# Kernel tuning notes

Measured on AMD Instinct MI355X. Metric: run time of the kernel, lower is better.

The kernel has to match this reference:

```python
import jax, jax.numpy as jnp
import numpy as np

VOCAB, EMB, HID, MAXLEN, BATCH = 32000, 256, 512, 64, 64


def setup_inputs() -> dict:
    key = jax.random.key(0)
    ks = jax.random.split(key, 12)
    s_e = 1.0 / np.sqrt(EMB)
    s_h = 1.0 / np.sqrt(HID)
    return {
        "encoder_h": jax.random.normal(ks[0], (1, BATCH, HID), jnp.float32),
        "encoder_c": jax.random.normal(ks[1], (1, BATCH, HID), jnp.float32),
        "target": jax.random.randint(ks[2], (BATCH, MAXLEN), 0, VOCAB, jnp.int64),
        "tf_mask": jax.random.randint(ks[3], (MAXLEN,), 0, 2, jnp.int32),
        "embedding": jax.random.normal(ks[4], (VOCAB, EMB), jnp.float32),
        "w_ih": jax.random.normal(ks[5], (4 * HID, EMB), jnp.float32) * s_e,
        "w_hh": jax.random.normal(ks[6], (4 * HID, HID), jnp.float32) * s_h,
        "b_ih": jax.random.normal(ks[7], (4 * HID,), jnp.float32) * s_h,
        "b_hh": jax.random.normal(ks[8], (4 * HID,), jnp.float32) * s_h,
        "fc_w": jax.random.normal(ks[9], (VOCAB, HID), jnp.float32) * s_h,
        "fc_b": jax.random.normal(ks[10], (VOCAB,), jnp.float32) * s_h,
        "target_length": 64,
    }


def reference(encoder_h, encoder_c, target, tf_mask, embedding, w_ih, w_hh,
              b_ih, b_hh, fc_w, fc_b, target_length):
    # encoder_h/c: [num_layers=1, B, H]; target: [B, T]; tf_mask: [T] (1 -> teacher forcing)
    B = target.shape[0]
    h0, c0 = encoder_h[0], encoder_c[0]              # [B, H]
    inp0 = jnp.zeros((B,), jnp.int32)                # SOS token id 0
    bias = b_ih + b_hh

    def step(carry, xs):
        h, c, inp = carry
        tgt_t, tf_t = xs
        x = embedding[inp]                           # [B, E] lookup
        gates = x @ w_ih.T + h @ w_hh.T + bias       # [B, 4H], PyTorch gate order i,f,g,o
        i, f, g, o = jnp.split(gates, 4, axis=-1)
        i, f, o = jax.nn.sigmoid(i), jax.nn.sigmoid(f), jax.nn.sigmoid(o)
        c = f * c + i * jnp.tanh(g)
        h = o * jnp.tanh(c)
        logits = h @ fc_w.T + fc_b                   # [B, V]
        greedy = jnp.argmax(logits, axis=-1).astype(jnp.int32)  # top-1 decode
        nxt = jnp.where(tf_t > 0, tgt_t, greedy)     # teacher forcing vs. greedy
        return (h, c, nxt), logits

    tgt_seq = target.T.astype(jnp.int32)             # [T, B]
    (h, c, _), outs = jax.lax.scan(step, (h0, c0, inp0), (tgt_seq, tf_mask))
    decoder_outputs = jnp.transpose(outs, (1, 0, 2))  # [B, T, V]
    return decoder_outputs, h[None], c[None]
```

## Files before the change

### kernel.cpp

```cpp
#include <hip/hip_runtime.h>
#include <cstdint>

#define VOCAB  32000
#define EMB    256
#define HID    512
#define TLEN   64
#define BATCH  64
#define G4     2048
#define OUT_LOGITS ((size_t)BATCH * TLEN * VOCAB)
#define BTV    ((size_t)TLEN * VOCAB)

typedef short s16x8 __attribute__((ext_vector_type(8)));
typedef float f32x4 __attribute__((ext_vector_type(4)));

#define WS_FCW_HI  0ull
#define WS_FCW_LO  32768000ull
#define WS_WIH_HI  65536000ull
#define WS_WIH_LO  66584576ull
#define WS_WHH_HI  67633152ull
#define WS_WHH_LO  69730304ull
#define WS_BIAS    71827456ull
#define WS_CBUF    71835648ull
#define WS_HBUF    71966720ull
#define WS_HHI     72097792ull
#define WS_HLO     76357632ull
#define WS_AMAX    80617472ull
#define WS_NEEDED  80650240ull

__device__ __forceinline__ unsigned bf16_hi_bits(float x) {
    unsigned u = __float_as_uint(x);
    return (u + 0x7FFFu + ((u >> 16) & 1u)) >> 16;
}
__device__ __forceinline__ float bf16_bits_to_f(unsigned b) {
    return __uint_as_float(b << 16);
}
__device__ __forceinline__ unsigned fkey(float x) {
    unsigned u = __float_as_uint(x);
    return (u & 0x80000000u) ? ~u : (u | 0x80000000u);
}

__global__ __launch_bounds__(256) void k_pre(
    const float* __restrict__ fcw, const float* __restrict__ wih, const float* __restrict__ whh,
    const float* __restrict__ bih, const float* __restrict__ bhh,
    const float* __restrict__ ench, const float* __restrict__ encc,
    unsigned short* fcw_hi, unsigned short* fcw_lo,
    unsigned short* wih_hi, unsigned short* wih_lo,
    unsigned short* whh_hi, unsigned short* whh_lo,
    float* bias, float* c_buf, unsigned short* hhi, unsigned short* hlo,
    unsigned long long* amax)
{
    size_t g = (size_t)blockIdx.x * 256 + threadIdx.x;
    size_t s = (size_t)gridDim.x * 256;
    for (size_t i = g; i < (size_t)VOCAB * HID; i += s) {
        float x = fcw[i]; unsigned hb = bf16_hi_bits(x);
        fcw_hi[i] = (unsigned short)hb;
        fcw_lo[i] = (unsigned short)bf16_hi_bits(x - bf16_bits_to_f(hb));
    }
    for (size_t i = g; i < (size_t)G4 * EMB; i += s) {
        float x = wih[i]; unsigned hb = bf16_hi_bits(x);
        wih_hi[i] = (unsigned short)hb;
        wih_lo[i] = (unsigned short)bf16_hi_bits(x - bf16_bits_to_f(hb));
    }
    for (size_t i = g; i < (size_t)G4 * HID; i += s) {
        float x = whh[i]; unsigned hb = bf16_hi_bits(x);
        whh_hi[i] = (unsigned short)hb;
        whh_lo[i] = (unsigned short)bf16_hi_bits(x - bf16_bits_to_f(hb));
    }
    for (size_t i = g; i < G4; i += s) bias[i] = bih[i] + bhh[i];
    for (size_t i = g; i < (size_t)BATCH * HID; i += s) {
        c_buf[i] = encc[i];
        float x = ench[i]; unsigned hb = bf16_hi_bits(x);
        hhi[i] = (unsigned short)hb;
        hlo[i] = (unsigned short)bf16_hi_bits(x - bf16_bits_to_f(hb));
    }
    for (size_t i = g; i < (size_t)TLEN * BATCH; i += s) amax[i] = 0ull;
}

__global__ __launch_bounds__(256) void k_cell(
    const float* __restrict__ emb,
    const unsigned short* __restrict__ wih_hi, const unsigned short* __restrict__ wih_lo,
    const unsigned short* __restrict__ whh_hi, const unsigned short* __restrict__ whh_lo,
    const float* __restrict__ bias,
    const int* __restrict__ target, const int* __restrict__ tf_mask,
    const unsigned long long* __restrict__ amax,
    float* c_buf, float* h_buf, unsigned short* hhi, unsigned short* hlo, int t)
{
    __shared__ __align__(16) unsigned short xs_hi[16 * 264];
    __shared__ __align__(16) unsigned short xs_lo[16 * 264];
    __shared__ float gbuf[4 * 16 * 16];
    __shared__ int tok_s[16];

    const int tid = threadIdx.x;
    const int jt = blockIdx.x >> 2;
    const int b0 = (blockIdx.x & 3) * 16;

    if (tid < 16) {
        int b = b0 + tid;
        int tok = 0;
        if (t > 0) {
            if (tf_mask[t - 1] > 0) tok = target[b * TLEN + (t - 1)];
            else {
                unsigned long long k = amax[(size_t)(t - 1) * BATCH + b];
                tok = (int)(~(unsigned)k);
            }
        }
        tok_s[tid] = tok;
    }
    __syncthreads();

    for (int i = tid; i < 16 * 32; i += 256) {
        int row = i >> 5, seg = i & 31;
        const float* src = emb + (size_t)tok_s[row] * EMB + seg * 8;
        int dst = row * 264 + seg * 8;
        #pragma unroll
        for (int e = 0; e < 8; e++) {
            float x = src[e]; unsigned hb = bf16_hi_bits(x);
            xs_hi[dst + e] = (unsigned short)hb;
            xs_lo[dst + e] = (unsigned short)bf16_hi_bits(x - bf16_bits_to_f(hb));
        }
    }
    __syncthreads();

    const int w = tid >> 6, l = tid & 63, li = l & 15, q = l >> 4;
    const int row0 = w * HID + jt * 16;
    const unsigned short* hh = hhi + (size_t)t * BATCH * HID;
    const unsigned short* hl = hlo + (size_t)t * BATCH * HID;

    f32x4 acc = {0.f, 0.f, 0.f, 0.f};
    #pragma unroll
    for (int kc = 0; kc < 8; kc++) {
        int ka = kc * 32 + q * 8;
        s16x8 ah = *(const s16x8*)(wih_hi + (size_t)(row0 + li) * EMB + ka);
        s16x8 al = *(const s16x8*)(wih_lo + (size_t)(row0 + li) * EMB + ka);
        s16x8 bh = *(const s16x8*)(xs_hi + li * 264 + ka);
        s16x8 bl = *(const s16x8*)(xs_lo + li * 264 + ka);
        acc = __builtin_amdgcn_mfma_f32_16x16x32_bf16(ah, bh, acc, 0, 0, 0);
        acc = __builtin_amdgcn_mfma_f32_16x16x32_bf16(ah, bl, acc, 0, 0, 0);
        acc = __builtin_amdgcn_mfma_f32_16x16x32_bf16(al, bh, acc, 0, 0, 0);
    }
    #pragma unroll
    for (int kc = 0; kc < 16; kc++) {
        int ka = kc * 32 + q * 8;
        s16x8 ah = *(const s16x8*)(whh_hi + (size_t)(row0 + li) * HID + ka);
        s16x8 al = *(const s16x8*)(whh_lo + (size_t)(row0 + li) * HID + ka);
        s16x8 bh = *(const s16x8*)(hh + (size_t)(b0 + li) * HID + ka);
        s16x8 bl = *(const s16x8*)(hl + (size_t)(b0 + li) * HID + ka);
        acc = __builtin_amdgcn_mfma_f32_16x16x32_bf16(ah, bh, acc, 0, 0, 0);
        acc = __builtin_amdgcn_mfma_f32_16x16x32_bf16(ah, bl, acc, 0, 0, 0);
        acc = __builtin_amdgcn_mfma_f32_16x16x32_bf16(al, bh, acc, 0, 0, 0);
    }
    #pragma unroll
    for (int r = 0; r < 4; r++) {
        int m = q * 4 + r;
        gbuf[w * 256 + m * 16 + li] = acc[r] + bias[row0 + m];
    }
    __syncthreads();

    {
        int jl = tid >> 4, bl = tid & 15;
        float gi = gbuf[0 * 256 + jl * 16 + bl];
        float gf = gbuf[1 * 256 + jl * 16 + bl];
        float gg = gbuf[2 * 256 + jl * 16 + bl];
        float go = gbuf[3 * 256 + jl * 16 + bl];
        int j = jt * 16 + jl, b = b0 + bl;
        size_t off = (size_t)b * HID + j;
        float ii = 1.f / (1.f + expf(-gi));
        float ff = 1.f / (1.f + expf(-gf));
        float oo = 1.f / (1.f + expf(-go));
        float c_new = ff * c_buf[off] + ii * tanhf(gg);
        float h_new = oo * tanhf(c_new);
        c_buf[off] = c_new;
        h_buf[off] = h_new;
        unsigned hb = bf16_hi_bits(h_new);
        size_t woff = (size_t)(t + 1) * BATCH * HID + off;
        hhi[woff] = (unsigned short)hb;
        hlo[woff] = (unsigned short)bf16_hi_bits(h_new - bf16_bits_to_f(hb));
    }
}

__global__ __launch_bounds__(256) void k_argmax(
    const unsigned short* __restrict__ fcw_hi, const unsigned short* __restrict__ fcw_lo,
    const unsigned short* __restrict__ hhi, const unsigned short* __restrict__ hlo,
    const float* __restrict__ fcb, const int* __restrict__ tf_mask,
    unsigned long long* __restrict__ amax_t, int t)
{
    if (tf_mask[t] > 0) return;

    __shared__ __align__(16) char smem[34816];
    unsigned short* sBh = (unsigned short*)smem;
    unsigned short* sBl = (unsigned short*)(smem + 17408);
    float* sOut = (float*)smem;

    const int tid = threadIdx.x;
    const int v0 = blockIdx.x * 64;
    const int w = tid >> 6, l = tid & 63, li = l & 15, q = l >> 4;
    const unsigned short* hh = hhi + (size_t)(t + 1) * BATCH * HID;
    const unsigned short* hl = hlo + (size_t)(t + 1) * BATCH * HID;

    f32x4 acc[4] = {{0,0,0,0},{0,0,0,0},{0,0,0,0},{0,0,0,0}};

    for (int kit = 0; kit < 4; kit++) {
        int kbase = kit * 128;
        __syncthreads();
        for (int i = tid; i < 1024; i += 256) {
            int row = i >> 4, seg = i & 15;
            *(s16x8*)(sBh + row * 136 + seg * 8) = *(const s16x8*)(hh + (size_t)row * HID + kbase + seg * 8);
            *(s16x8*)(sBl + row * 136 + seg * 8) = *(const s16x8*)(hl + (size_t)row * HID + kbase + seg * 8);
        }
        __syncthreads();
        #pragma unroll
        for (int kc = 0; kc < 4; kc++) {
            int ka = kbase + kc * 32 + q * 8;
            int kl = kc * 32 + q * 8;
            s16x8 ah = *(const s16x8*)(fcw_hi + (size_t)(v0 + w * 16 + li) * HID + ka);
            s16x8 al = *(const s16x8*)(fcw_lo + (size_t)(v0 + w * 16 + li) * HID + ka);
            #pragma unroll
            for (int bt = 0; bt < 4; bt++) {
                s16x8 bh = *(const s16x8*)(sBh + (bt * 16 + li) * 136 + kl);
                s16x8 bl = *(const s16x8*)(sBl + (bt * 16 + li) * 136 + kl);
                acc[bt] = __builtin_amdgcn_mfma_f32_16x16x32_bf16(ah, bh, acc[bt], 0, 0, 0);
                acc[bt] = __builtin_amdgcn_mfma_f32_16x16x32_bf16(ah, bl, acc[bt], 0, 0, 0);
                acc[bt] = __builtin_amdgcn_mfma_f32_16x16x32_bf16(al, bh, acc[bt], 0, 0, 0);
            }
        }
    }
    __syncthreads();

    #pragma unroll
    for (int bt = 0; bt < 4; bt++) {
        #pragma unroll
        for (int r = 0; r < 4; r++) {
            int vl = w * 16 + q * 4 + r;
            int b = bt * 16 + li;
            sOut[b * 68 + vl] = acc[bt][r] + fcb[v0 + vl];
        }
    }
    __syncthreads();

    {
        int b = tid >> 2, i4 = tid & 3;
        float best = -1e38f; int bidx = 0;
        #pragma unroll
        for (int e = 0; e < 16; e++) {
            int vl = i4 * 16 + e;
            float x = sOut[b * 68 + vl];
            if (x > best) { best = x; bidx = vl; }
        }
        unsigned long long pk = ((unsigned long long)fkey(best) << 32) | (unsigned)(~(unsigned)(v0 + bidx));
        unsigned long long o1 = __shfl_xor(pk, 1); if (o1 > pk) pk = o1;
        unsigned long long o2 = __shfl_xor(pk, 2); if (o2 > pk) pk = o2;
        if (i4 == 0) atomicMax(amax_t + b, pk);
    }
}

__global__ __launch_bounds__(512) void k_blogits(
    const unsigned short* __restrict__ fcw_hi, const unsigned short* __restrict__ fcw_lo,
    const unsigned short* __restrict__ hhi, const unsigned short* __restrict__ hlo,
    const float* __restrict__ fcb, float* __restrict__ out)
{
    __shared__ __align__(16) char smem[67584];
    unsigned short* sBh = (unsigned short*)smem;
    unsigned short* sBl = (unsigned short*)(smem + 32768);
    float* sOut = (float*)smem;

    const int tid = threadIdx.x;
    const int mt = blockIdx.x & 15;
    const int nt = blockIdx.x >> 4;
    const int n0 = nt * 256;
    const int ww = tid >> 6, l = tid & 63, li = l & 15, q = l >> 4;
    const int wm = ww >> 2, wn = ww & 3;
    const size_t hbase = ((size_t)mt * 256 + BATCH) * HID;

    f32x4 acc[8][4];
    #pragma unroll
    for (int i = 0; i < 8; i++)
        #pragma unroll
        for (int j = 0; j < 4; j++) acc[i][j] = (f32x4){0.f, 0.f, 0.f, 0.f};

    for (int kit = 0; kit < 8; kit++) {
        int kbase = kit * 64;
        __syncthreads();
        #pragma unroll
        for (int i2 = 0; i2 < 4; i2++) {
            int idx = i2 * 512 + tid;
            int row = idx >> 3, c8 = idx & 7;
            size_t src = hbase + (size_t)row * HID + kbase + c8 * 8;
            int dst = row * 64 + ((c8 ^ (row & 7)) << 3);
            *(s16x8*)(sBh + dst) = *(const s16x8*)(hhi + src);
            *(s16x8*)(sBl + dst) = *(const s16x8*)(hlo + src);
        }
        __syncthreads();
        #pragma unroll
        for (int kc = 0; kc < 2; kc++) {
            int ka = kbase + kc * 32 + q * 8;
            s16x8 ah[4], al[4];
            #pragma unroll
            for (int nf = 0; nf < 4; nf++) {
                size_t arow = (size_t)(n0 + wn * 64 + nf * 16 + li) * HID + ka;
                ah[nf] = *(const s16x8*)(fcw_hi + arow);
                al[nf] = *(const s16x8*)(fcw_lo + arow);
            }
            #pragma unroll
            for (int mf = 0; mf < 8; mf++) {
                int row = wm * 128 + mf * 16 + li;
                int ch = kc * 4 + q;
                int off = row * 64 + (((ch ^ (row & 7)) & 7) << 3);
                s16x8 bh = *(const s16x8*)(sBh + off);
                s16x8 bl = *(const s16x8*)(sBl + off);
                #pragma unroll
                for (int nf = 0; nf < 4; nf++) {
                    acc[mf][nf] = __builtin_amdgcn_mfma_f32_16x16x32_bf16(ah[nf], bh, acc[mf][nf], 0, 0, 0);
                    acc[mf][nf] = __builtin_amdgcn_mfma_f32_16x16x32_bf16(ah[nf], bl, acc[mf][nf], 0, 0, 0);
                    acc[mf][nf] = __builtin_amdgcn_mfma_f32_16x16x32_bf16(al[nf], bh, acc[mf][nf], 0, 0, 0);
                }
            }
        }
    }

    for (int rd = 0; rd < 4; rd++) {
        __syncthreads();
        if (wm == (rd >> 1)) {
            #pragma unroll
            for (int mfi = 0; mfi < 4; mfi++) {
                int mf = (rd & 1) * 4 + mfi;
                int mrow = mf * 16 + li - (rd & 1) * 64;
                #pragma unroll
                for (int nf = 0; nf < 4; nf++) {
                    #pragma unroll
                    for (int r = 0; r < 4; r++) {
                        int nl = wn * 64 + nf * 16 + q * 4 + r;
                        sOut[mrow * 264 + nl] = acc[mf][nf][r] + fcb[n0 + nl];
                    }
                }
            }
        }
        __syncthreads();
        int tglob = mt * 4 + rd;
        #pragma unroll
        for (int it = 0; it < 8; it++) {
            int idx = it * 512 + tid;
            int row = idx >> 6, v4 = idx & 63;
            float4 val = *(const float4*)&sOut[row * 264 + v4 * 4];
            *(float4*)(out + (size_t)row * BTV + (size_t)tglob * VOCAB + n0 + v4 * 4) = val;
        }
    }
}

__global__ __launch_bounds__(256) void k_tail(const float* __restrict__ h_buf,
                                              const float* __restrict__ c_buf,
                                              float* __restrict__ out)
{
    int i = blockIdx.x * 256 + threadIdx.x;
    if (i < BATCH * HID) out[OUT_LOGITS + i] = h_buf[i];
    else                 out[OUT_LOGITS + i] = c_buf[i - BATCH * HID];
}

extern "C" void kernel_launch(void* const* d_in, const int* in_sizes, int n_in,
                              void* d_out, int out_size, void* d_ws, size_t ws_size,
                              hipStream_t stream) {
    const float* ench   = (const float*)d_in[0];
    const float* encc   = (const float*)d_in[1];
    const int*   target = (const int*)d_in[2];
    const int*   tfmask = (const int*)d_in[3];
    const float* emb    = (const float*)d_in[4];
    const float* wih    = (const float*)d_in[5];
    const float* whh    = (const float*)d_in[6];
    const float* bih    = (const float*)d_in[7];
    const float* bhh    = (const float*)d_in[8];
    const float* fcw    = (const float*)d_in[9];
    const float* fcb    = (const float*)d_in[10];

    if (ws_size < WS_NEEDED) return;

    char* ws = (char*)d_ws;
    unsigned short* fcw_hi = (unsigned short*)(ws + WS_FCW_HI);
    unsigned short* fcw_lo = (unsigned short*)(ws + WS_FCW_LO);
    unsigned short* wih_hi = (unsigned short*)(ws + WS_WIH_HI);
    unsigned short* wih_lo = (unsigned short*)(ws + WS_WIH_LO);
    unsigned short* whh_hi = (unsigned short*)(ws + WS_WHH_HI);
    unsigned short* whh_lo = (unsigned short*)(ws + WS_WHH_LO);
    float* bias  = (float*)(ws + WS_BIAS);
    float* c_buf = (float*)(ws + WS_CBUF);
    float* h_buf = (float*)(ws + WS_HBUF);
    unsigned short* hhi = (unsigned short*)(ws + WS_HHI);
    unsigned short* hlo = (unsigned short*)(ws + WS_HLO);
    unsigned long long* amax = (unsigned long long*)(ws + WS_AMAX);
    float* out = (float*)d_out;

    k_pre<<<4096, 256, 0, stream>>>(fcw, wih, whh, bih, bhh, ench, encc,
                                    fcw_hi, fcw_lo, wih_hi, wih_lo, whh_hi, whh_lo,
                                    bias, c_buf, hhi, hlo, amax);

    for (int t = 0; t < TLEN; t++) {
        k_cell<<<128, 256, 0, stream>>>(emb, wih_hi, wih_lo, whh_hi, whh_lo, bias,
                                        target, tfmask, amax, c_buf, h_buf, hhi, hlo, t);
        if (t < TLEN - 1)
            k_argmax<<<500, 256, 0, stream>>>(fcw_hi, fcw_lo, hhi, hlo, fcb, tfmask,
                                              amax + (size_t)t * BATCH, t);
    }

    k_blogits<<<2000, 512, 0, stream>>>(fcw_hi, fcw_lo, hhi, hlo, fcb, out);

    k_tail<<<256, 256, 0, stream>>>(h_buf, c_buf, out);
}
```

Baseline: 2.914 ms.

## Drop LDS staging in argmax, double-buffer blogits via direct global-to-LDS loads

k_argmax no longer stages h through shared memory. Each wave now reads its own 16 batch rows straight from global and covers all 64 vocab columns, which removes the per-k-tile barriers. k_blogits double-buffers the h tiles in 128KB of LDS using global_load_lds async copies, so the next tile streams in while MFMAs consume the current one. It also remaps block IDs so blocks sharing an fc_w tile are spread across XCDs. The 128KB LDS footprint limits each CU to one block, and the loop now depends on correct barrier placement around the async copies.

```diff
diff --git a/kernel.cpp b/kernel.cpp
--- a/kernel.cpp
+++ b/kernel.cpp
@@ -37,6 +37,11 @@
 __device__ __forceinline__ unsigned fkey(float x) {
     unsigned u = __float_as_uint(x);
     return (u & 0x80000000u) ? ~u : (u | 0x80000000u);
+}
+__device__ __forceinline__ void gload_lds16(const void* g, void* l) {
+    __builtin_amdgcn_global_load_lds(
+        (const __attribute__((address_space(1))) void*)g,
+        (__attribute__((address_space(3))) void*)l, 16, 0, 0);
 }
 
 __global__ __launch_bounds__(256) void k_pre(
@@ -186,53 +191,42 @@
 {
     if (tf_mask[t] > 0) return;
 
-    __shared__ __align__(16) char smem[34816];
-    unsigned short* sBh = (unsigned short*)smem;
-    unsigned short* sBl = (unsigned short*)(smem + 17408);
-    float* sOut = (float*)smem;
+    __shared__ __align__(16) float sOut[64 * 68];
 
     const int tid = threadIdx.x;
     const int v0 = blockIdx.x * 64;
     const int w = tid >> 6, l = tid & 63, li = l & 15, q = l >> 4;
     const unsigned short* hh = hhi + (size_t)(t + 1) * BATCH * HID;
     const unsigned short* hl = hlo + (size_t)(t + 1) * BATCH * HID;
+    const int brow = w * 16 + li;
 
     f32x4 acc[4] = {{0,0,0,0},{0,0,0,0},{0,0,0,0},{0,0,0,0}};
 
-    for (int kit = 0; kit < 4; kit++) {
-        int kbase = kit * 128;
-        __syncthreads();
-        for (int i = tid; i < 1024; i += 256) {
-            int row = i >> 4, seg = i & 15;
-            *(s16x8*)(sBh + row * 136 + seg * 8) = *(const s16x8*)(hh + (size_t)row * HID + kbase + seg * 8);
-            *(s16x8*)(sBl + row * 136 + seg * 8) = *(const s16x8*)(hl + (size_t)row * HID + kbase + seg * 8);
-        }
-        __syncthreads();
-        #pragma unroll
-        for (int kc = 0; kc < 4; kc++) {
-            int ka = kbase + kc * 32 + q * 8;
-            int kl = kc * 32 + q * 8;
-            s16x8 ah = *(const s16x8*)(fcw_hi + (size_t)(v0 + w * 16 + li) * HID + ka);
-            s16x8 al = *(const s16x8*)(fcw_lo + (size_t)(v0 + w * 16 + li) * HID + ka);
-            #pragma unroll
-            for (int bt = 0; bt < 4; bt++) {
-                s16x8 bh = *(const s16x8*)(sBh + (bt * 16 + li) * 136 + kl);
-                s16x8 bl = *(const s16x8*)(sBl + (bt * 16 + li) * 136 + kl);
-                acc[bt] = __builtin_amdgcn_mfma_f32_16x16x32_bf16(ah, bh, acc[bt], 0, 0, 0);
-                acc[bt] = __builtin_amdgcn_mfma_f32_16x16x32_bf16(ah, bl, acc[bt], 0, 0, 0);
-                acc[bt] = __builtin_amdgcn_mfma_f32_16x16x32_bf16(al, bh, acc[bt], 0, 0, 0);
-            }
-        }
-    }
-    __syncthreads();
-
-    #pragma unroll
-    for (int bt = 0; bt < 4; bt++) {
+    #pragma unroll
+    for (int kc = 0; kc < 16; kc++) {
+        int ka = kc * 32 + q * 8;
+        s16x8 bh = *(const s16x8*)(hh + (size_t)brow * HID + ka);
+        s16x8 bl = *(const s16x8*)(hl + (size_t)brow * HID + ka);
+        s16x8 ah[4], al[4];
+        #pragma unroll
+        for (int nf = 0; nf < 4; nf++) {
+            ah[nf] = *(const s16x8*)(fcw_hi + (size_t)(v0 + nf * 16 + li) * HID + ka);
+            al[nf] = *(const s16x8*)(fcw_lo + (size_t)(v0 + nf * 16 + li) * HID + ka);
+        }
+        #pragma unroll
+        for (int nf = 0; nf < 4; nf++) {
+            acc[nf] = __builtin_amdgcn_mfma_f32_16x16x32_bf16(ah[nf], bh, acc[nf], 0, 0, 0);
+            acc[nf] = __builtin_amdgcn_mfma_f32_16x16x32_bf16(ah[nf], bl, acc[nf], 0, 0, 0);
+            acc[nf] = __builtin_amdgcn_mfma_f32_16x16x32_bf16(al[nf], bh, acc[nf], 0, 0, 0);
+        }
+    }
+
+    #pragma unroll
+    for (int nf = 0; nf < 4; nf++) {
         #pragma unroll
         for (int r = 0; r < 4; r++) {
-            int vl = w * 16 + q * 4 + r;
-            int b = bt * 16 + li;
-            sOut[b * 68 + vl] = acc[bt][r] + fcb[v0 + vl];
+            int vl = nf * 16 + q * 4 + r;
+            sOut[brow * 68 + vl] = acc[nf][r] + fcb[v0 + vl];
         }
     }
     __syncthreads();
@@ -258,14 +252,13 @@
     const unsigned short* __restrict__ hhi, const unsigned short* __restrict__ hlo,
     const float* __restrict__ fcb, float* __restrict__ out)
 {
-    __shared__ __align__(16) char smem[67584];
-    unsigned short* sBh = (unsigned short*)smem;
-    unsigned short* sBl = (unsigned short*)(smem + 32768);
+    __shared__ __align__(16) char smem[131072];
     float* sOut = (float*)smem;
 
     const int tid = threadIdx.x;
-    const int mt = blockIdx.x & 15;
-    const int nt = blockIdx.x >> 4;
+    const int bid = ((int)blockIdx.x & 7) * 250 + ((int)blockIdx.x >> 3);
+    const int mt = bid & 15;
+    const int nt = bid >> 4;
     const int n0 = nt * 256;
     const int ww = tid >> 6, l = tid & 63, li = l & 15, q = l >> 4;
     const int wm = ww >> 2, wn = ww & 3;
@@ -277,19 +270,30 @@
         #pragma unroll
         for (int j = 0; j < 4; j++) acc[i][j] = (f32x4){0.f, 0.f, 0.f, 0.f};
 
+    auto STAGE = [&](int buf, int kit2) {
+        unsigned short* dBh = (unsigned short*)(smem + buf * 65536);
+        unsigned short* dBl = (unsigned short*)(smem + buf * 65536 + 32768);
+        int kbase = kit2 * 64;
+        #pragma unroll
+        for (int i = 0; i < 4; i++) {
+            int idx = i * 512 + tid;
+            int row = idx >> 3, c8 = idx & 7;
+            int sc = (c8 ^ (row & 7)) << 3;
+            size_t src = hbase + (size_t)row * HID + kbase + sc;
+            gload_lds16(hhi + src, dBh + idx * 8);
+            gload_lds16(hlo + src, dBl + idx * 8);
+        }
+    };
+
+    STAGE(0, 0);
+    __syncthreads();
+
     for (int kit = 0; kit < 8; kit++) {
+        const int cur = kit & 1;
+        if (kit < 7) STAGE(cur ^ 1, kit + 1);
+        const unsigned short* sBh = (const unsigned short*)(smem + cur * 65536);
+        const unsigned short* sBl = (const unsigned short*)(smem + cur * 65536 + 32768);
         int kbase = kit * 64;
-        __syncthreads();
-        #pragma unroll
-        for (int i2 = 0; i2 < 4; i2++) {
-            int idx = i2 * 512 + tid;
-            int row = idx >> 3, c8 = idx & 7;
-            size_t src = hbase + (size_t)row * HID + kbase + c8 * 8;
-            int dst = row * 64 + ((c8 ^ (row & 7)) << 3);
-            *(s16x8*)(sBh + dst) = *(const s16x8*)(hhi + src);
-            *(s16x8*)(sBl + dst) = *(const s16x8*)(hlo + src);
-        }
-        __syncthreads();
         #pragma unroll
         for (int kc = 0; kc < 2; kc++) {
             int ka = kbase + kc * 32 + q * 8;
@@ -315,6 +319,7 @@
                 }
             }
         }
+        __syncthreads();
     }
 
     for (int rd = 0; rd < 4; rd++) {
```

Result: slower. 3.629 ms (+24.5%).
